# Kernel optimization log

Measured on AMD Instinct MI355X. Metric: run time of the kernel, lower is better.

The kernel has to match this reference:

```python
import jax, jax.numpy as jnp
import numpy as np

TEACHER_BOX = (-0.9, 0.9, -0.9, 0.9)  # x1, x2, y1, y2
STUDENT_BOX = (-0.8, 0.8, -0.8, 0.8)
STUDENT_TEMP = 0.1
TEACHER_TEMP = 0.04


def _box_grids(t_box, s_box, H, W):
    # Faithful to DINOLoss.box_to_grid: grid size derives from the TEACHER box,
    # meshgrid stacked as (y, x) -- torch quirk replicated (grid_sample reads ch0 as x).
    x1, x2, y1, y2 = t_box
    gW = int(abs(x1 - x2) / 2 * W)
    gH = int(abs(y1 - y2) / 2 * H)
    ty, tx = jnp.linspace(y1, y2, gH), jnp.linspace(x1, x2, gW)
    tgrid = jnp.stack(jnp.meshgrid(ty, tx, indexing='ij'), axis=-1)  # [gH, gW, 2]
    x1, x2, y1, y2 = s_box
    sy, sx = jnp.linspace(y1, y2, gH), jnp.linspace(x1, x2, gW)
    sgrid = jnp.stack(jnp.meshgrid(sy, sx, indexing='ij'), axis=-1)  # [gH, gW, 2]
    return tgrid, sgrid


def grid_sample_border(feat, grid):
    # feat: [B, C, H, W]; grid: [gh, gw, 2]; torch convention: grid[...,0]->x, grid[...,1]->y
    # bilinear, align_corners=False, padding_mode='border'
    B, C, H, W = feat.shape
    gx, gy = grid[..., 0], grid[..., 1]
    ix = jnp.clip(((gx + 1.0) * W - 1.0) * 0.5, 0.0, W - 1.0)
    iy = jnp.clip(((gy + 1.0) * H - 1.0) * 0.5, 0.0, H - 1.0)
    ix0 = jnp.floor(ix).astype(jnp.int32)
    iy0 = jnp.floor(iy).astype(jnp.int32)
    ix1 = jnp.clip(ix0 + 1, 0, W - 1)
    iy1 = jnp.clip(iy0 + 1, 0, H - 1)
    ix0 = jnp.clip(ix0, 0, W - 1)
    iy0 = jnp.clip(iy0, 0, H - 1)
    wx = ix - ix0
    wy = iy - iy0
    v00 = feat[:, :, iy0, ix0]  # [B, C, gh, gw]
    v01 = feat[:, :, iy0, ix1]
    v10 = feat[:, :, iy1, ix0]
    v11 = feat[:, :, iy1, ix1]
    return (v00 * (1 - wy) * (1 - wx) + v01 * (1 - wy) * wx
            + v10 * wy * (1 - wx) + v11 * wy * wx)


def setup_inputs() -> dict:
    key = jax.random.key(0)
    k1, k2, k3 = jax.random.split(key, 3)
    teacher_feat = jax.random.normal(k1, (8, 8192, 28, 28), dtype=jnp.float32)
    student_feat = jax.random.normal(k2, (8, 8192, 12, 12), dtype=jnp.float32)
    center = jax.random.normal(k3, (1, 8192), dtype=jnp.float32)
    return {"teacher_feat": teacher_feat, "student_feat": student_feat, "center": center}


def reference(teacher_feat, student_feat, center):
    H, W = teacher_feat.shape[-2:]
    tgrid, sgrid = _box_grids(TEACHER_BOX, STUDENT_BOX, H, W)
    # teacher: centered + sharpened softmax over channel dim (detached in original)
    t_prob = jax.nn.softmax((teacher_feat - center[:, :, None, None]) / TEACHER_TEMP, axis=1)
    t_common = jax.lax.stop_gradient(grid_sample_border(t_prob, tgrid))  # [B, C, gh, gw]
    s_common = grid_sample_border(student_feat / STUDENT_TEMP, sgrid)    # [B, C, gh, gw]
    loss = (-t_common * jax.nn.log_softmax(s_common, axis=1)).sum(axis=1).mean()
    return loss
```

## Files before the change

### kernel.cpp

```cpp
#include <hip/hip_runtime.h>
#include <hip/hip_bf16.h>

typedef __attribute__((ext_vector_type(8))) short  short8;
typedef __attribute__((ext_vector_type(4))) float  float4v;
typedef __attribute__((ext_vector_type(4))) unsigned short ushort4v;

#define NC    8192
#define TPIX  784
#define NB    8

#define WS_M2    0
#define WS_ZACC  262144
#define WS_DACC  287232
#define WS_ZPOS  312320
#define WS_ZERO_OFF 262144
#define WS_ZERO_LEN 70176

__device__ __forceinline__ unsigned short bf16rne(float f) {
    unsigned int u = __float_as_uint(f);
    u = (u + 0x7FFFu + ((u >> 16) & 1u)) >> 16;
    return (unsigned short)u;
}

__device__ __forceinline__ short8 cvt8(float4v a, float4v b) {
    union { __hip_bfloat162 h[4]; short8 s; } u;
    u.h[0] = __float22bfloat162_rn(float2{a[0], a[1]});
    u.h[1] = __float22bfloat162_rn(float2{a[2], a[3]});
    u.h[2] = __float22bfloat162_rn(float2{b[0], b[1]});
    u.h[3] = __float22bfloat162_rn(float2{b[2], b[3]});
    return u.s;
}

__global__ void k_init_m2(unsigned short* __restrict__ m2) {
    int p  = blockIdx.x;
    int sp = threadIdx.x;
    int y = p / 28, x = p % 28;
    float val = 0.f;
    if (sp < 144) {
        int v = sp / 12, u = sp % 12;
        float kyv = 0.f, kxu = 0.f;
        for (int a = 0; a < 25; ++a) {
            float ctc = 0.9f + 1.05f * (float)a;
            int   i0  = (int)ctc; float wt = ctc - (float)i0;
            float Ay  = (i0 == y) ? (1.f - wt) : ((i0 + 1 == y) ? wt : 0.f);
            float Ax  = (i0 == x) ? (1.f - wt) : ((i0 + 1 == x) ? wt : 0.f);
            float csc = 0.7f + 0.4f * (float)a;
            int   j0  = (int)csc; float wsv = csc - (float)j0;
            float Bv  = (j0 == v) ? (1.f - wsv) : ((j0 + 1 == v) ? wsv : 0.f);
            float Bu  = (j0 == u) ? (1.f - wsv) : ((j0 + 1 == u) ? wsv : 0.f);
            kyv += Ay * Bv;
            kxu += Ax * Bu;
        }
        val = 10.f * kyv * kxu;
    }
    m2[p * 160 + sp] = bf16rne(val);
}

__launch_bounds__(256, 3)
__global__ void k_main(const float* __restrict__ teacher,
                       const float* __restrict__ student,
                       const float* __restrict__ center,
                       const unsigned short* __restrict__ m2,
                       float* __restrict__ zacc, float* __restrict__ dacc) {
    const int b  = blockIdx.z;
    const int cg = blockIdx.y;
    const int t  = threadIdx.x;
    const int w    = t >> 6;
    const int lane = t & 63;
    const int l15  = lane & 15;
    const int g    = lane >> 4;

    const int tile0 = (blockIdx.x * 4 + w) * 2;
    const bool va = (tile0     < 49);
    const bool vb = (tile0 + 1 < 49);
    const int p0a = va ? tile0 * 16 : 0;
    const int p0b = vb ? (tile0 + 1) * 16 : 0;

    short8 afa[5], afb[5];
    {
        const unsigned short* ra = m2 + (p0a + l15) * 160;
        const unsigned short* rb = m2 + (p0b + l15) * 160;
        #pragma unroll
        for (int ks = 0; ks < 5; ++ks) {
            afa[ks] = *(const short8*)(ra + ks * 32 + g * 8);
            afb[ks] = *(const short8*)(rb + ks * 32 + g * 8);
        }
    }

    float sEa[4] = {0.f, 0.f, 0.f, 0.f}, sEYa[4] = {0.f, 0.f, 0.f, 0.f};
    float sEb[4] = {0.f, 0.f, 0.f, 0.f}, sEYb[4] = {0.f, 0.f, 0.f, 0.f};

    const long long sbase = (long long)(b * NC) * 144;
    const long long tbase = (long long)(b * NC) * TPIX;
    const short8 zfrag = {0, 0, 0, 0, 0, 0, 0, 0};

    for (int cc = 0; cc < 32; ++cc) {
        const int c = cg * 512 + cc * 16 + l15;
        const float* srow = student + sbase + (long long)c * 144;

        short8 bf[5];
        #pragma unroll
        for (int ks = 0; ks < 4; ++ks)
            bf[ks] = cvt8(*(const float4v*)(srow + ks * 32 + g * 8),
                          *(const float4v*)(srow + ks * 32 + g * 8 + 4));
        bf[4] = (g < 2) ? cvt8(*(const float4v*)(srow + 128 + g * 8),
                               *(const float4v*)(srow + 128 + g * 8 + 4))
                        : zfrag;

        const float cen = center[c];
        const float* trow = teacher + tbase + (long long)c * TPIX;

        {
            float4v tv = *(const float4v*)(trow + p0a + 4 * g);
            float4v acc = {0.f, 0.f, 0.f, 0.f};
            #pragma unroll
            for (int ks = 0; ks < 5; ++ks)
                acc = __builtin_amdgcn_mfma_f32_16x16x32_bf16(afa[ks], bf[ks], acc, 0, 0, 0);
            #pragma unroll
            for (int i = 0; i < 4; ++i) {
                float e = exp2f(fmaf(36.0673762f, tv[i] - cen, -233.7165966f));
                sEa[i] += e;
                sEYa[i] = fmaf(e, acc[i], sEYa[i]);
            }
        }
        {
            float4v tv = *(const float4v*)(trow + p0b + 4 * g);
            float4v acc = {0.f, 0.f, 0.f, 0.f};
            #pragma unroll
            for (int ks = 0; ks < 5; ++ks)
                acc = __builtin_amdgcn_mfma_f32_16x16x32_bf16(afb[ks], bf[ks], acc, 0, 0, 0);
            #pragma unroll
            for (int i = 0; i < 4; ++i) {
                float e = exp2f(fmaf(36.0673762f, tv[i] - cen, -233.7165966f));
                sEb[i] += e;
                sEYb[i] = fmaf(e, acc[i], sEYb[i]);
            }
        }
    }

    #pragma unroll
    for (int i = 0; i < 4; ++i) {
        float e0 = sEa[i], y0 = sEYa[i], e1 = sEb[i], y1 = sEYb[i];
        e0 += __shfl_xor(e0, 1); e0 += __shfl_xor(e0, 2); e0 += __shfl_xor(e0, 4); e0 += __shfl_xor(e0, 8);
        y0 += __shfl_xor(y0, 1); y0 += __shfl_xor(y0, 2); y0 += __shfl_xor(y0, 4); y0 += __shfl_xor(y0, 8);
        e1 += __shfl_xor(e1, 1); e1 += __shfl_xor(e1, 2); e1 += __shfl_xor(e1, 4); e1 += __shfl_xor(e1, 8);
        y1 += __shfl_xor(y1, 1); y1 += __shfl_xor(y1, 2); y1 += __shfl_xor(y1, 4); y1 += __shfl_xor(y1, 8);
        if (l15 == 0) {
            if (va) {
                atomicAdd(zacc + b * TPIX + p0a + 4 * g + i, e0);
                atomicAdd(dacc + b * TPIX + p0a + 4 * g + i, y0);
            }
            if (vb) {
                atomicAdd(zacc + b * TPIX + p0b + 4 * g + i, e1);
                atomicAdd(dacc + b * TPIX + p0b + 4 * g + i, y1);
            }
        }
    }
}

__launch_bounds__(256)
__global__ void k_lse(const float* __restrict__ student, float* __restrict__ zpos) {
    const int cg = blockIdx.x;
    const int a  = blockIdx.y;
    const int b  = blockIdx.z;
    const int t  = threadIdx.x;

    const float cv = 0.7f + 0.4f * (float)a;
    const int   v0 = (int)cv;
    const float wv = cv - (float)v0;
    const float W0 = 10.f * (1.f - wv), W1 = 10.f * wv;

    float accs[25];
    #pragma unroll
    for (int p = 0; p < 25; ++p) accs[p] = 0.f;

    for (int j = 0; j < 8; ++j) {
        const int c = cg * 2048 + 256 * j + t;
        const float* row = student + (long long)(b * NC + c) * 144 + v0 * 12;
        float4v r0 = *(const float4v*)(row + 0);
        float4v r1 = *(const float4v*)(row + 4);
        float4v r2 = *(const float4v*)(row + 8);
        float4v s0 = *(const float4v*)(row + 12);
        float4v s1 = *(const float4v*)(row + 16);
        float4v s2 = *(const float4v*)(row + 20);

        float R[12];
        #pragma unroll
        for (int u = 0; u < 4; ++u) {
            R[u]     = fmaf(W0, r0[u], W1 * s0[u]);
            R[u + 4] = fmaf(W0, r1[u], W1 * s1[u]);
            R[u + 8] = fmaf(W0, r2[u], W1 * s2[u]);
        }
        #pragma unroll
        for (int p = 0; p < 25; ++p) {
            const float cu = 0.7f + 0.4f * (float)p;
            const int   u0 = (int)cu;
            const float wu = cu - (float)u0;
            float sc = fmaf(1.f - wu, R[u0], wu * R[u0 + 1]);
            accs[p] += exp2f(fmaf(1.44269504f, sc, -86.5617025f));
        }
    }

    #pragma unroll
    for (int p = 0; p < 25; ++p) {
        float v = accs[p];
        #pragma unroll
        for (int m = 1; m < 64; m <<= 1) v += __shfl_xor(v, m);
        accs[p] = v;
    }
    if ((t & 63) == 0) {
        #pragma unroll
        for (int p = 0; p < 25; ++p)
            atomicAdd(zpos + (b * 25 + a) * 25 + p, accs[p]);
    }
}

__global__ void k_final(const float* __restrict__ zacc, const float* __restrict__ dacc,
                        const float* __restrict__ zpos, float* __restrict__ out) {
    __shared__ float red[8];
    int t = threadIdx.x;
    float s = 0.f;
    for (int i = t; i < 5000; i += 256) s += 60.f + logf(zpos[i]);
    for (int i = t; i < NB * TPIX; i += 256) s -= dacc[i] / zacc[i];
    for (int m = 1; m < 64; m <<= 1) s += __shfl_xor(s, m);
    if ((t & 63) == 0) red[t >> 6] = s;
    __syncthreads();
    if (t == 0) out[0] = (red[0] + red[1] + red[2] + red[3]) * (1.f / 5000.f);
}

extern "C" void kernel_launch(void* const* d_in, const int* in_sizes, int n_in,
                              void* d_out, int out_size, void* d_ws, size_t ws_size,
                              hipStream_t stream) {
    const float* teacher = (const float*)d_in[0];
    const float* student = (const float*)d_in[1];
    const float* center  = (const float*)d_in[2];

    char* ws = (char*)d_ws;
    unsigned short* m2 = (unsigned short*)(ws + WS_M2);
    float* zacc = (float*)(ws + WS_ZACC);
    float* dacc = (float*)(ws + WS_DACC);
    float* zpos = (float*)(ws + WS_ZPOS);

    hipMemsetAsync(ws + WS_ZERO_OFF, 0, WS_ZERO_LEN, stream);
    k_init_m2<<<784, 160, 0, stream>>>(m2);
    k_main<<<dim3(7, 16, 8), 256, 0, stream>>>(teacher, student, center, m2, zacc, dacc);
    k_lse<<<dim3(4, 25, 8), 256, 0, stream>>>(student, zpos);
    k_final<<<1, 256, 0, stream>>>(zacc, dacc, zpos, (float*)d_out);
}
```

Baseline: 170.8 us.

## Stage teacher tiles into LDS via async global-to-LDS DMA with triple buffering

The main kernel now uses 512-thread blocks that each cover 256 teacher pixels and 256 channels. Teacher rows are streamed into a triple-buffered, XOR-swizzled LDS tile with global_load_lds, issued two iterations ahead, so loads are coalesced and overlap the MFMA and exp work. The last partial pixel tile (pixels 768-783) moves to a separate tail kernel. This replaces strided per-lane global teacher loads, at the cost of 48KB of LDS per block, barriers every iteration, and an extra launch.

New measurement: 168.1 us. Within noise of the previous version (-1.6%).

```diff
diff --git a/kernel.cpp b/kernel.cpp
--- a/kernel.cpp
+++ b/kernel.cpp
@@ -29,6 +29,12 @@
     u.h[2] = __float22bfloat162_rn(float2{b[0], b[1]});
     u.h[3] = __float22bfloat162_rn(float2{b[2], b[3]});
     return u.s;
+}
+
+__device__ __forceinline__ void dma16(const float* g, float* l) {
+    __builtin_amdgcn_global_load_lds(
+        (const __attribute__((address_space(1))) unsigned int*)g,
+        (__attribute__((address_space(3))) unsigned int*)l, 16, 0, 0);
 }
 
 __global__ void k_init_m2(unsigned short* __restrict__ m2) {
@@ -56,30 +62,29 @@
     m2[p * 160 + sp] = bf16rne(val);
 }
 
-__launch_bounds__(256, 3)
+__launch_bounds__(512, 2)
 __global__ void k_main(const float* __restrict__ teacher,
                        const float* __restrict__ student,
                        const float* __restrict__ center,
                        const unsigned short* __restrict__ m2,
                        float* __restrict__ zacc, float* __restrict__ dacc) {
+    __shared__ float tlds[3][4096];
+
     const int b  = blockIdx.z;
     const int cg = blockIdx.y;
+    const int ph = blockIdx.x;
     const int t  = threadIdx.x;
-    const int w    = t >> 6;
-    const int lane = t & 63;
-    const int l15  = lane & 15;
-    const int g    = lane >> 4;
-
-    const int tile0 = (blockIdx.x * 4 + w) * 2;
-    const bool va = (tile0     < 49);
-    const bool vb = (tile0 + 1 < 49);
-    const int p0a = va ? tile0 * 16 : 0;
-    const int p0b = vb ? (tile0 + 1) * 16 : 0;
-
+    const int w = t >> 6, lane = t & 63, l15 = lane & 15, g = lane >> 4;
+
+    const long long tbase = (long long)(b * NC) * TPIX;
+    const long long sbase = (long long)(b * NC) * 144;
+    const int c0 = cg * 256;
+
+    const int Ta = ph * 16 + 2 * w;
     short8 afa[5], afb[5];
     {
-        const unsigned short* ra = m2 + (p0a + l15) * 160;
-        const unsigned short* rb = m2 + (p0b + l15) * 160;
+        const unsigned short* ra = m2 + (Ta * 16 + l15) * 160;
+        const unsigned short* rb = m2 + ((Ta + 1) * 16 + l15) * 160;
         #pragma unroll
         for (int ks = 0; ks < 5; ++ks) {
             afa[ks] = *(const short8*)(ra + ks * 32 + g * 8);
@@ -87,54 +92,84 @@
         }
     }
 
-    float sEa[4] = {0.f, 0.f, 0.f, 0.f}, sEYa[4] = {0.f, 0.f, 0.f, 0.f};
-    float sEb[4] = {0.f, 0.f, 0.f, 0.f}, sEYb[4] = {0.f, 0.f, 0.f, 0.f};
-
-    const long long sbase = (long long)(b * NC) * 144;
-    const long long tbase = (long long)(b * NC) * TPIX;
-    const short8 zfrag = {0, 0, 0, 0, 0, 0, 0, 0};
-
-    for (int cc = 0; cc < 32; ++cc) {
-        const int c = cg * 512 + cc * 16 + l15;
-        const float* srow = student + sbase + (long long)c * 144;
+    const int ch0 = w, ch1 = w + 8;
+    const float* tsrc0 = teacher + tbase + (long long)(c0 + ch0) * TPIX + ph * 256 + ((lane ^ (ch0 & 7)) << 2);
+    const float* tsrc1 = teacher + tbase + (long long)(c0 + ch1) * TPIX + ph * 256 + ((lane ^ (ch1 & 7)) << 2);
+    const long long cstep = 16LL * TPIX;
+
+    float sEa[4] = {0.f,0.f,0.f,0.f}, sEYa[4] = {0.f,0.f,0.f,0.f};
+    float sEb[4] = {0.f,0.f,0.f,0.f}, sEYb[4] = {0.f,0.f,0.f,0.f};
+    const short8 zfrag = {0,0,0,0,0,0,0,0};
+
+    dma16(tsrc0,             &tlds[0][ch0 * 256]);
+    dma16(tsrc1,             &tlds[0][ch1 * 256]);
+    dma16(tsrc0 + cstep,     &tlds[1][ch0 * 256]);
+    dma16(tsrc1 + cstep,     &tlds[1][ch1 * 256]);
+
+    for (int cc = 0; cc < 16; ++cc) {
+        __builtin_amdgcn_s_barrier();
+        const int cbase = c0 + cc * 16;
+        const float* srow = student + sbase + (long long)(cbase + l15) * 144;
+
+        float4v s0 = *(const float4v*)(srow + 0);
+        float4v s1 = *(const float4v*)(srow + 4);
+        float4v s2 = *(const float4v*)(srow + 32 + 0);
+        float4v s3 = *(const float4v*)(srow + 32 + 4);
+        float4v s4 = *(const float4v*)(srow + 64 + 0);
+        float4v s5 = *(const float4v*)(srow + 64 + 4);
+        float4v s6 = *(const float4v*)(srow + 96 + 0);
+        float4v s7 = *(const float4v*)(srow + 96 + 4);
+        float4v s8 = {0.f,0.f,0.f,0.f}, s9 = {0.f,0.f,0.f,0.f};
+        if (g < 2) {
+            s8 = *(const float4v*)(srow + 128 + 0);
+            s9 = *(const float4v*)(srow + 128 + 4);
+        }
+        const float cen = center[cbase + l15];
+
+        __builtin_amdgcn_sched_barrier(0);
+        {
+            const int ccn = (cc + 2 < 16) ? cc + 2 : 15;
+            const int bw2 = (cc + 2) % 3;
+            dma16(tsrc0 + (long long)ccn * cstep, &tlds[bw2][ch0 * 256]);
+            dma16(tsrc1 + (long long)ccn * cstep, &tlds[bw2][ch1 * 256]);
+        }
+        __builtin_amdgcn_sched_barrier(0);
 
         short8 bf[5];
-        #pragma unroll
-        for (int ks = 0; ks < 4; ++ks)
-            bf[ks] = cvt8(*(const float4v*)(srow + ks * 32 + g * 8),
-                          *(const float4v*)(srow + ks * 32 + g * 8 + 4));
-        bf[4] = (g < 2) ? cvt8(*(const float4v*)(srow + 128 + g * 8),
-                               *(const float4v*)(srow + 128 + g * 8 + 4))
-                        : zfrag;
-
-        const float cen = center[c];
-        const float* trow = teacher + tbase + (long long)c * TPIX;
-
-        {
-            float4v tv = *(const float4v*)(trow + p0a + 4 * g);
-            float4v acc = {0.f, 0.f, 0.f, 0.f};
-            #pragma unroll
-            for (int ks = 0; ks < 5; ++ks)
-                acc = __builtin_amdgcn_mfma_f32_16x16x32_bf16(afa[ks], bf[ks], acc, 0, 0, 0);
-            #pragma unroll
-            for (int i = 0; i < 4; ++i) {
-                float e = exp2f(fmaf(36.0673762f, tv[i] - cen, -233.7165966f));
-                sEa[i] += e;
-                sEYa[i] = fmaf(e, acc[i], sEYa[i]);
-            }
-        }
-        {
-            float4v tv = *(const float4v*)(trow + p0b + 4 * g);
-            float4v acc = {0.f, 0.f, 0.f, 0.f};
-            #pragma unroll
-            for (int ks = 0; ks < 5; ++ks)
-                acc = __builtin_amdgcn_mfma_f32_16x16x32_bf16(afb[ks], bf[ks], acc, 0, 0, 0);
-            #pragma unroll
-            for (int i = 0; i < 4; ++i) {
-                float e = exp2f(fmaf(36.0673762f, tv[i] - cen, -233.7165966f));
-                sEb[i] += e;
-                sEYb[i] = fmaf(e, acc[i], sEYb[i]);
-            }
+        bf[0] = cvt8(s0, s1);
+        bf[1] = cvt8(s2, s3);
+        bf[2] = cvt8(s4, s5);
+        bf[3] = cvt8(s6, s7);
+        bf[4] = (g < 2) ? cvt8(s8, s9) : zfrag;
+
+        float4v acca = {0.f,0.f,0.f,0.f}, accb = {0.f,0.f,0.f,0.f};
+        #pragma unroll
+        for (int ks = 0; ks < 5; ++ks) {
+            acca = __builtin_amdgcn_mfma_f32_16x16x32_bf16(afa[ks], bf[ks], acca, 0, 0, 0);
+            accb = __builtin_amdgcn_mfma_f32_16x16x32_bf16(afb[ks], bf[ks], accb, 0, 0, 0);
+        }
+
+        __builtin_amdgcn_sched_barrier(0);
+        asm volatile("s_waitcnt vmcnt(2)" ::: "memory");
+        __builtin_amdgcn_sched_barrier(0);
+        __builtin_amdgcn_s_barrier();
+        __builtin_amdgcn_sched_barrier(0);
+
+        const int br = cc % 3;
+        const float* Tp = &tlds[br][l15 * 256];
+        const int qa = (2 * w)     * 4 + g;
+        const int qb = (2 * w + 1) * 4 + g;
+        float4v tva = *(const float4v*)(Tp + (((qa ^ (l15 & 7)) << 2)));
+        float4v tvb = *(const float4v*)(Tp + (((qb ^ (l15 & 7)) << 2)));
+
+        #pragma unroll
+        for (int i = 0; i < 4; ++i) {
+            float ea = exp2f(fmaf(36.0673762f, tva[i] - cen, -233.7165966f));
+            sEa[i] += ea;
+            sEYa[i] = fmaf(ea, acca[i], sEYa[i]);
+            float eb = exp2f(fmaf(36.0673762f, tvb[i] - cen, -233.7165966f));
+            sEb[i] += eb;
+            sEYb[i] = fmaf(eb, accb[i], sEYb[i]);
         }
     }
 
@@ -146,14 +181,65 @@
         e1 += __shfl_xor(e1, 1); e1 += __shfl_xor(e1, 2); e1 += __shfl_xor(e1, 4); e1 += __shfl_xor(e1, 8);
         y1 += __shfl_xor(y1, 1); y1 += __shfl_xor(y1, 2); y1 += __shfl_xor(y1, 4); y1 += __shfl_xor(y1, 8);
         if (l15 == 0) {
-            if (va) {
-                atomicAdd(zacc + b * TPIX + p0a + 4 * g + i, e0);
-                atomicAdd(dacc + b * TPIX + p0a + 4 * g + i, y0);
-            }
-            if (vb) {
-                atomicAdd(zacc + b * TPIX + p0b + 4 * g + i, e1);
-                atomicAdd(dacc + b * TPIX + p0b + 4 * g + i, y1);
-            }
+            atomicAdd(zacc + b * TPIX + Ta * 16 + 4 * g + i, e0);
+            atomicAdd(dacc + b * TPIX + Ta * 16 + 4 * g + i, y0);
+            atomicAdd(zacc + b * TPIX + (Ta + 1) * 16 + 4 * g + i, e1);
+            atomicAdd(dacc + b * TPIX + (Ta + 1) * 16 + 4 * g + i, y1);
+        }
+    }
+}
+
+__launch_bounds__(256, 4)
+__global__ void k_tail(const float* __restrict__ teacher,
+                       const float* __restrict__ student,
+                       const float* __restrict__ center,
+                       const unsigned short* __restrict__ m2,
+                       float* __restrict__ zacc, float* __restrict__ dacc) {
+    const int b   = blockIdx.y;
+    const int cgi = blockIdx.x;
+    const int t   = threadIdx.x;
+    const int w = t >> 6, lane = t & 63, l15 = lane & 15, g = lane >> 4;
+
+    short8 af[5];
+    #pragma unroll
+    for (int ks = 0; ks < 5; ++ks)
+        af[ks] = *(const short8*)(m2 + (768 + l15) * 160 + ks * 32 + g * 8);
+
+    float sE[4] = {0.f,0.f,0.f,0.f}, sEY[4] = {0.f,0.f,0.f,0.f};
+    const short8 zfrag = {0,0,0,0,0,0,0,0};
+
+    for (int cc = 0; cc < 8; ++cc) {
+        const int c = cgi * 512 + cc * 64 + w * 16 + l15;
+        const float* srow = student + (long long)(b * NC + c) * 144;
+        short8 bf[5];
+        #pragma unroll
+        for (int ks = 0; ks < 4; ++ks)
+            bf[ks] = cvt8(*(const float4v*)(srow + ks * 32),
+                          *(const float4v*)(srow + ks * 32 + 4));
+        bf[4] = (g < 2) ? cvt8(*(const float4v*)(srow + 128),
+                               *(const float4v*)(srow + 128 + 4)) : zfrag;
+        const float cen = center[c];
+        float4v tv = *(const float4v*)(teacher + (long long)(b * NC + c) * TPIX + 768 + 4 * g);
+        float4v acc = {0.f,0.f,0.f,0.f};
+        #pragma unroll
+        for (int ks = 0; ks < 5; ++ks)
+            acc = __builtin_amdgcn_mfma_f32_16x16x32_bf16(af[ks], bf[ks], acc, 0, 0, 0);
+        #pragma unroll
+        for (int i = 0; i < 4; ++i) {
+            float e = exp2f(fmaf(36.0673762f, tv[i] - cen, -233.7165966f));
+            sE[i] += e;
+            sEY[i] = fmaf(e, acc[i], sEY[i]);
+        }
+    }
+
+    #pragma unroll
+    for (int i = 0; i < 4; ++i) {
+        float e = sE[i], y = sEY[i];
+        e += __shfl_xor(e, 1); e += __shfl_xor(e, 2); e += __shfl_xor(e, 4); e += __shfl_xor(e, 8);
+        y += __shfl_xor(y, 1); y += __shfl_xor(y, 2); y += __shfl_xor(y, 4); y += __shfl_xor(y, 8);
+        if (l15 == 0) {
+            atomicAdd(zacc + b * TPIX + 768 + 4 * g + i, e);
+            atomicAdd(dacc + b * TPIX + 768 + 4 * g + i, y);
         }
     }
 }
@@ -243,7 +329,8 @@
 
     hipMemsetAsync(ws + WS_ZERO_OFF, 0, WS_ZERO_LEN, stream);
     k_init_m2<<<784, 160, 0, stream>>>(m2);
-    k_main<<<dim3(7, 16, 8), 256, 0, stream>>>(teacher, student, center, m2, zacc, dacc);
+    k_main<<<dim3(3, 32, 8), 512, 0, stream>>>(teacher, student, center, m2, zacc, dacc);
+    k_tail<<<dim3(16, 8), 256, 0, stream>>>(teacher, student, center, m2, zacc, dacc);
     k_lse<<<dim3(4, 25, 8), 256, 0, stream>>>(student, zpos);
     k_final<<<1, 256, 0, stream>>>(zacc, dacc, zpos, (float*)d_out);
 }
```

## Pre-convert student features to bf16 and process two channel groups per iteration

Applied to the files above, without the earlier changes.

Adds a pre-pass kernel that converts student rows to padded bf16 and precomputes per-channel exponent offsets, so the main kernel loads ready-made MFMA fragments instead of converting fp32 per tile. The main loop now handles two 16-channel groups per iteration with four independent MFMA chains. The grid doubles in the channel dimension and the occupancy hint drops from 3 to 2 blocks. This costs an extra kernel launch and about 20MB of workspace traffic, and falls back to the old inline path when the workspace is too small.

New measurement: 156.0 us. -8.7%, faster.

```diff
diff --git a/kernel.cpp b/kernel.cpp
--- a/kernel.cpp
+++ b/kernel.cpp
@@ -10,11 +10,14 @@
 #define NB    8
 
 #define WS_M2    0
-#define WS_ZACC  262144
-#define WS_DACC  287232
-#define WS_ZPOS  312320
-#define WS_ZERO_OFF 262144
+#define WS_O     250880
+#define WS_ZACC  283648
+#define WS_DACC  308736
+#define WS_ZPOS  333824
+#define WS_ZERO_OFF WS_ZACC
 #define WS_ZERO_LEN 70176
+#define WS_STUDB 360448
+#define WS_NEED  (360448 + 65536*320)
 
 __device__ __forceinline__ unsigned short bf16rne(float f) {
     unsigned int u = __float_as_uint(f);
@@ -56,19 +59,34 @@
     m2[p * 160 + sp] = bf16rne(val);
 }
 
-__launch_bounds__(256, 3)
+__launch_bounds__(256)
+__global__ void k_pre(const float* __restrict__ student, const float* __restrict__ center,
+                      unsigned short* __restrict__ studb, float* __restrict__ o) {
+    const int tid = blockIdx.x * 256 + threadIdx.x;
+    const int row = tid / 20, ch = tid % 20;
+    short8 hv = {0,0,0,0,0,0,0,0};
+    if (ch < 18) {
+        const float* src = student + (long long)row * 144 + ch * 8;
+        hv = cvt8(*(const float4v*)(src), *(const float4v*)(src + 4));
+    }
+    *(short8*)(studb + (long long)row * 160 + ch * 8) = hv;
+    if (ch == 0 && row < NC)
+        o[row] = fmaf(36.0673762f, center[row], 233.7165966f);
+}
+
+template<bool PRE>
+__launch_bounds__(256, 2)
 __global__ void k_main(const float* __restrict__ teacher,
                        const float* __restrict__ student,
                        const float* __restrict__ center,
                        const unsigned short* __restrict__ m2,
+                       const unsigned short* __restrict__ studb,
+                       const float* __restrict__ o,
                        float* __restrict__ zacc, float* __restrict__ dacc) {
     const int b  = blockIdx.z;
     const int cg = blockIdx.y;
     const int t  = threadIdx.x;
-    const int w    = t >> 6;
-    const int lane = t & 63;
-    const int l15  = lane & 15;
-    const int g    = lane >> 4;
+    const int w = t >> 6, lane = t & 63, l15 = lane & 15, g = lane >> 4;
 
     const int tile0 = (blockIdx.x * 4 + w) * 2;
     const bool va = (tile0     < 49);
@@ -87,54 +105,74 @@
         }
     }
 
-    float sEa[4] = {0.f, 0.f, 0.f, 0.f}, sEYa[4] = {0.f, 0.f, 0.f, 0.f};
-    float sEb[4] = {0.f, 0.f, 0.f, 0.f}, sEYb[4] = {0.f, 0.f, 0.f, 0.f};
-
+    float sEa[4] = {0.f,0.f,0.f,0.f}, sEYa[4] = {0.f,0.f,0.f,0.f};
+    float sEb[4] = {0.f,0.f,0.f,0.f}, sEYb[4] = {0.f,0.f,0.f,0.f};
+
+    const long long tbase = (long long)(b * NC) * TPIX;
     const long long sbase = (long long)(b * NC) * 144;
-    const long long tbase = (long long)(b * NC) * TPIX;
-    const short8 zfrag = {0, 0, 0, 0, 0, 0, 0, 0};
-
-    for (int cc = 0; cc < 32; ++cc) {
-        const int c = cg * 512 + cc * 16 + l15;
-        const float* srow = student + sbase + (long long)c * 144;
-
-        short8 bf[5];
-        #pragma unroll
-        for (int ks = 0; ks < 4; ++ks)
-            bf[ks] = cvt8(*(const float4v*)(srow + ks * 32 + g * 8),
-                          *(const float4v*)(srow + ks * 32 + g * 8 + 4));
-        bf[4] = (g < 2) ? cvt8(*(const float4v*)(srow + 128 + g * 8),
-                               *(const float4v*)(srow + 128 + g * 8 + 4))
-                        : zfrag;
-
-        const float cen = center[c];
-        const float* trow = teacher + tbase + (long long)c * TPIX;
-
-        {
-            float4v tv = *(const float4v*)(trow + p0a + 4 * g);
-            float4v acc = {0.f, 0.f, 0.f, 0.f};
+    const short8 zfrag = {0,0,0,0,0,0,0,0};
+
+    for (int cc = 0; cc < 8; ++cc) {
+        const int cA = cg * 256 + cc * 32 + l15;
+        const int cB = cA + 16;
+
+        short8 bfA[5], bfB[5];
+        float oA, oB;
+        if (PRE) {
+            const unsigned short* rA = studb + ((long long)(b * NC) + cA) * 160;
+            const unsigned short* rB = rA + 16 * 160;
             #pragma unroll
-            for (int ks = 0; ks < 5; ++ks)
-                acc = __builtin_amdgcn_mfma_f32_16x16x32_bf16(afa[ks], bf[ks], acc, 0, 0, 0);
+            for (int ks = 0; ks < 5; ++ks) {
+                bfA[ks] = *(const short8*)(rA + ks * 32 + g * 8);
+                bfB[ks] = *(const short8*)(rB + ks * 32 + g * 8);
+            }
+            oA = o[cA];
+            oB = o[cB];
+        } else {
+            const float* sA = student + sbase + (long long)cA * 144;
+            const float* sB = sA + 16 * 144;
             #pragma unroll
-            for (int i = 0; i < 4; ++i) {
-                float e = exp2f(fmaf(36.0673762f, tv[i] - cen, -233.7165966f));
-                sEa[i] += e;
-                sEYa[i] = fmaf(e, acc[i], sEYa[i]);
-            }
-        }
-        {
-            float4v tv = *(const float4v*)(trow + p0b + 4 * g);
-            float4v acc = {0.f, 0.f, 0.f, 0.f};
-            #pragma unroll
-            for (int ks = 0; ks < 5; ++ks)
-                acc = __builtin_amdgcn_mfma_f32_16x16x32_bf16(afb[ks], bf[ks], acc, 0, 0, 0);
-            #pragma unroll
-            for (int i = 0; i < 4; ++i) {
-                float e = exp2f(fmaf(36.0673762f, tv[i] - cen, -233.7165966f));
-                sEb[i] += e;
-                sEYb[i] = fmaf(e, acc[i], sEYb[i]);
-            }
+            for (int ks = 0; ks < 4; ++ks) {
+                bfA[ks] = cvt8(*(const float4v*)(sA + ks * 32 + g * 8),
+                               *(const float4v*)(sA + ks * 32 + g * 8 + 4));
+                bfB[ks] = cvt8(*(const float4v*)(sB + ks * 32 + g * 8),
+                               *(const float4v*)(sB + ks * 32 + g * 8 + 4));
+            }
+            bfA[4] = (g < 2) ? cvt8(*(const float4v*)(sA + 128 + g * 8),
+                                    *(const float4v*)(sA + 128 + g * 8 + 4)) : zfrag;
+            bfB[4] = (g < 2) ? cvt8(*(const float4v*)(sB + 128 + g * 8),
+                                    *(const float4v*)(sB + 128 + g * 8 + 4)) : zfrag;
+            oA = fmaf(36.0673762f, center[cA], 233.7165966f);
+            oB = fmaf(36.0673762f, center[cB], 233.7165966f);
+        }
+
+        const float* trA = teacher + tbase + (long long)cA * TPIX;
+        const float* trB = trA + 16LL * TPIX;
+        float4v tvAa = *(const float4v*)(trA + p0a + 4 * g);
+        float4v tvAb = *(const float4v*)(trA + p0b + 4 * g);
+        float4v tvBa = *(const float4v*)(trB + p0a + 4 * g);
+        float4v tvBb = *(const float4v*)(trB + p0b + 4 * g);
+
+        float4v accAa = {0.f,0.f,0.f,0.f}, accAb = {0.f,0.f,0.f,0.f};
+        float4v accBa = {0.f,0.f,0.f,0.f}, accBb = {0.f,0.f,0.f,0.f};
+        #pragma unroll
+        for (int ks = 0; ks < 5; ++ks) {
+            accAa = __builtin_amdgcn_mfma_f32_16x16x32_bf16(afa[ks], bfA[ks], accAa, 0, 0, 0);
+            accAb = __builtin_amdgcn_mfma_f32_16x16x32_bf16(afb[ks], bfA[ks], accAb, 0, 0, 0);
+            accBa = __builtin_amdgcn_mfma_f32_16x16x32_bf16(afa[ks], bfB[ks], accBa, 0, 0, 0);
+            accBb = __builtin_amdgcn_mfma_f32_16x16x32_bf16(afb[ks], bfB[ks], accBb, 0, 0, 0);
+        }
+
+        #pragma unroll
+        for (int i = 0; i < 4; ++i) {
+            float e0 = exp2f(fmaf(36.0673762f, tvAa[i], -oA));
+            sEa[i] += e0;  sEYa[i] = fmaf(e0, accAa[i], sEYa[i]);
+            float e1 = exp2f(fmaf(36.0673762f, tvAb[i], -oA));
+            sEb[i] += e1;  sEYb[i] = fmaf(e1, accAb[i], sEYb[i]);
+            float e2 = exp2f(fmaf(36.0673762f, tvBa[i], -oB));
+            sEa[i] += e2;  sEYa[i] = fmaf(e2, accBa[i], sEYa[i]);
+            float e3 = exp2f(fmaf(36.0673762f, tvBb[i], -oB));
+            sEb[i] += e3;  sEYb[i] = fmaf(e3, accBb[i], sEYb[i]);
         }
     }
 
@@ -236,14 +274,24 @@
     const float* center  = (const float*)d_in[2];
 
     char* ws = (char*)d_ws;
-    unsigned short* m2 = (unsigned short*)(ws + WS_M2);
-    float* zacc = (float*)(ws + WS_ZACC);
-    float* dacc = (float*)(ws + WS_DACC);
-    float* zpos = (float*)(ws + WS_ZPOS);
+    unsigned short* m2    = (unsigned short*)(ws + WS_M2);
+    float*          oarr  = (float*)(ws + WS_O);
+    float*          zacc  = (float*)(ws + WS_ZACC);
+    float*          dacc  = (float*)(ws + WS_DACC);
+    float*          zpos  = (float*)(ws + WS_ZPOS);
+    unsigned short* studb = (unsigned short*)(ws + WS_STUDB);
 
     hipMemsetAsync(ws + WS_ZERO_OFF, 0, WS_ZERO_LEN, stream);
     k_init_m2<<<784, 160, 0, stream>>>(m2);
-    k_main<<<dim3(7, 16, 8), 256, 0, stream>>>(teacher, student, center, m2, zacc, dacc);
+
+    if (ws_size >= (size_t)WS_NEED) {
+        k_pre<<<5120, 256, 0, stream>>>(student, center, studb, oarr);
+        k_main<true><<<dim3(7, 32, 8), 256, 0, stream>>>(teacher, student, center, m2,
+                                                         studb, oarr, zacc, dacc);
+    } else {
+        k_main<false><<<dim3(7, 32, 8), 256, 0, stream>>>(teacher, student, center, m2,
+                                                          studb, oarr, zacc, dacc);
+    }
     k_lse<<<dim3(4, 25, 8), 256, 0, stream>>>(student, zpos);
     k_final<<<1, 256, 0, stream>>>(zacc, dacc, zpos, (float*)d_out);
 }
```
